# Optimization experiments

Measured on AMD Instinct MI355X. Metric: run time of the kernel, lower is better.

## Reference

```python
import jax, jax.numpy as jnp
import numpy as np

N_NODES = 50000


def gcn_conv(x, src, dst, W, b, n):
    # PyG GCNConv: h = x @ W; out[i] = sum_j norm_ij * h[j] + b, with added self-loops
    h = x @ W  # [N, out]
    deg = jax.ops.segment_sum(jnp.ones_like(dst, dtype=h.dtype), dst, num_segments=n)
    inv_sqrt_deg = jnp.where(deg > 0, jax.lax.rsqrt(deg), 0.0)  # [N]
    coeff = inv_sqrt_deg[src] * inv_sqrt_deg[dst]  # [E]
    msg = h[src] * coeff[:, None]  # [E, out] gather (memory-bound)
    out = jax.ops.segment_sum(msg, dst, num_segments=n)  # scatter-add
    return out + b


def setup_inputs() -> dict:
    key = jax.random.key(0)
    ks = jax.random.split(key, 8)
    n, e, c_in, c_hid, c_out = N_NODES, 800000, 128, 128, 64
    x = jax.random.normal(ks[0], (n, c_in), dtype=jnp.float32)
    edge_index = jax.random.randint(ks[1], (2, e), 0, n, dtype=jnp.int64)
    # Glorot-ish scaled weights
    W1 = jax.random.normal(ks[2], (c_in, c_hid), dtype=jnp.float32) / np.sqrt(c_in)
    b1 = jnp.zeros((c_hid,), dtype=jnp.float32)
    W2 = jax.random.normal(ks[3], (c_hid, c_out), dtype=jnp.float32) / np.sqrt(c_hid)
    b2 = jnp.zeros((c_out,), dtype=jnp.float32)
    lin_W = jax.random.normal(ks[4], (2 * c_out, c_out), dtype=jnp.float32) / np.sqrt(2 * c_out)
    lin_b = jnp.zeros((c_out,), dtype=jnp.float32)
    return {"x": x, "edge_index": edge_index, "W1": W1, "b1": b1,
            "W2": W2, "b2": b2, "lin_W": lin_W, "lin_b": lin_b}


def reference(x, edge_index, W1, b1, W2, b2, lin_W, lin_b):
    n = x.shape[0]
    # add self-loops (as GCNConv does by default)
    loops = jnp.arange(n, dtype=edge_index.dtype)
    src = jnp.concatenate([edge_index[0], loops])
    dst = jnp.concatenate([edge_index[1], loops])

    def branch(x):
        h = jax.nn.relu(gcn_conv(x, src, dst, W1, b1, n))
        # dropout: identity in eval mode (training=False)
        return gcn_conv(h, src, dst, W2, b2, n)

    x1 = branch(x)
    x2 = branch(x)
    # FusionMethod == 'Concat'
    fused = jnp.concatenate([x1, x2], axis=1) @ lin_W + lin_b
    return jax.nn.log_softmax(fused, axis=1)
```

## Files before the change

### kernel.cpp

```cpp
#include <hip/hip_runtime.h>


#define CIN  128
#define CHID 128
#define COUT 64
#define BCAP_SH 13
#define BCAP    (1 << BCAP_SH)
#define BINCHUNK 2048

typedef short v8s __attribute__((ext_vector_type(8)));
typedef float v4f __attribute__((ext_vector_type(4)));

static __device__ __forceinline__ unsigned short f2bf(float f) {
    unsigned int u = __float_as_uint(f);
    unsigned int r = (u + 0x7fffu + ((u >> 16) & 1u)) >> 16;
    return (unsigned short)r;
}
static __device__ __forceinline__ float bf2f(unsigned short v) {
    return __uint_as_float(((unsigned int)v) << 16);
}

__global__ __launch_bounds__(256) void bin_kernel(const int* __restrict__ src,
                                                  const int* __restrict__ dst,
                                                  int* __restrict__ bcursor,
                                                  unsigned int* __restrict__ binned, int E) {
    __shared__ int h[256];
    __shared__ int base[256];
    int t = threadIdx.x;
    h[t] = 0;
    __syncthreads();
    int e0 = blockIdx.x * BINCHUNK;
    int e1 = e0 + BINCHUNK; if (e1 > E) e1 = E;
    for (int e = e0 + t; e < e1; e += 256)
        atomicAdd(&h[dst[e] >> 8], 1);
    __syncthreads();
    int c = h[t];
    base[t] = (t << BCAP_SH) + (c ? atomicAdd(&bcursor[t], c) : 0);
    __syncthreads();
    h[t] = 0;
    __syncthreads();
    for (int e = e0 + t; e < e1; e += 256) {
        int d = dst[e];
        int b = d >> 8;
        int pos = base[b] + atomicAdd(&h[b], 1);
        binned[pos] = (unsigned int)src[e] | (((unsigned int)d & 255u) << 16);
    }
}

__global__ __launch_bounds__(512) void csr_kernel(const unsigned int* __restrict__ binned,
                                                  const int* __restrict__ bcursor,
                                                  int2* __restrict__ rowpair,
                                                  float* __restrict__ inv,
                                                  int* __restrict__ ebuf, int n) {
    __shared__ int h[256];
    __shared__ int s[256];
    int b = blockIdx.x;
    int t = threadIdx.x;
    int base = b << BCAP_SH;
    int cnt  = bcursor[b];
    if (t < 256) h[t] = 0;
    __syncthreads();
    for (int i = t; i < cnt; i += 512)
        atomicAdd(&h[binned[base + i] >> 16], 1);
    __syncthreads();
    int myc = (t < 256) ? h[t] : 0;
    if (t < 256) s[t] = myc;
    __syncthreads();
    for (int off = 1; off < 256; off <<= 1) {
        int u = (t >= off && t < 256) ? s[t - off] : 0;
        __syncthreads();
        if (t < 256) s[t] += u;
        __syncthreads();
    }
    if (t < 256) {
        int excl = s[t] - myc;
        int node = (b << 8) + t;
        if (node < n) {
            rowpair[node] = make_int2(base + excl, base + excl + myc);
            inv[node] = rsqrtf((float)(myc + 1));
        }
        h[t] = base + excl;
    }
    __syncthreads();
    for (int i = t; i < cnt; i += 512) {
        unsigned int v = binned[base + i];
        int pos = atomicAdd(&h[v >> 16], 1);
        ebuf[pos] = (int)(v & 0xffffu);
    }
}

__global__ __launch_bounds__(128) void wprep_kernel(const float* __restrict__ W1,
                                                    const float* __restrict__ W2,
                                                    const float* __restrict__ b2,
                                                    const float* __restrict__ linW,
                                                    const float* __restrict__ linb,
                                                    unsigned short* __restrict__ Wt1,
                                                    unsigned short* __restrict__ Wt2,
                                                    float* __restrict__ bp,
                                                    int* __restrict__ bcursor) {
    int b = blockIdx.x;
    int t = threadIdx.x;
    if (b < CHID) {
        Wt1[b * CIN + t] = f2bf(W1[t * CHID + b]);
        if (t < COUT) {
            float acc = 0.f;
#pragma unroll 8
            for (int k = 0; k < COUT; ++k) {
                float wsv = linW[k * COUT + t] + linW[(k + COUT) * COUT + t];
                acc = fmaf(W2[b * COUT + k], wsv, acc);
            }
            Wt2[t * CHID + b] = f2bf(acc);
        }
    } else {
        bcursor[t] = 0;
        bcursor[128 + t] = 0;
        if (t < COUT) {
            float acc = 0.f;
#pragma unroll 8
            for (int k = 0; k < COUT; ++k) {
                float wsv = linW[k * COUT + t] + linW[(k + COUT) * COUT + t];
                acc = fmaf(b2[k], wsv, acc);
            }
            bp[t] = acc + linb[t];
        }
    }
}

template <int NOUT, bool A_BF16>
__global__ __launch_bounds__(256) void gemm_mfma(const void* __restrict__ Aptr,
                                                 const unsigned short* __restrict__ Wt,
                                                 const float* __restrict__ inv,
                                                 unsigned short* __restrict__ H, int n) {
    constexpr int NCT = NOUT / 16;
    int lane = threadIdx.x & 63;
    int wave = threadIdx.x >> 6;
    int quad = lane >> 4, r16 = lane & 15;
    int row0 = (blockIdx.x * 4 + wave) * 16;
    if (row0 >= n) return;
    int arow = row0 + r16;
    if (arow >= n) arow = n - 1;

    v4f acc[NCT];
#pragma unroll
    for (int c = 0; c < NCT; ++c) acc[c] = (v4f){0.f, 0.f, 0.f, 0.f};

#pragma unroll
    for (int kc = 0; kc < 4; ++kc) {
        v8s af;
        if (A_BF16) {
            const unsigned short* A = (const unsigned short*)Aptr;
            af = *(const v8s*)(A + (size_t)arow * 128 + kc * 32 + quad * 8);
        } else {
            const float* A = (const float*)Aptr;
            const float4* ap = (const float4*)(A + (size_t)arow * 128 + kc * 32 + quad * 8);
            float4 a0 = ap[0], a1 = ap[1];
            af[0] = (short)f2bf(a0.x); af[1] = (short)f2bf(a0.y);
            af[2] = (short)f2bf(a0.z); af[3] = (short)f2bf(a0.w);
            af[4] = (short)f2bf(a1.x); af[5] = (short)f2bf(a1.y);
            af[6] = (short)f2bf(a1.z); af[7] = (short)f2bf(a1.w);
        }
#pragma unroll
        for (int ct = 0; ct < NCT; ++ct) {
            v8s bf = *(const v8s*)(Wt + (size_t)(ct * 16 + r16) * 128 + kc * 32 + quad * 8);
            acc[ct] = __builtin_amdgcn_mfma_f32_16x16x32_bf16(af, bf, acc[ct], 0, 0, 0);
        }
    }

    float4 iv = ((const float4*)(inv + row0))[quad];
#pragma unroll
    for (int ct = 0; ct < NCT; ++ct) {
#pragma unroll
        for (int i = 0; i < 4; ++i) {
            int orow = row0 + quad * 4 + i;
            if (orow < n) {
                float sc = (i == 0) ? iv.x : (i == 1) ? iv.y : (i == 2) ? iv.z : iv.w;
                H[(size_t)orow * NOUT + ct * 16 + r16] = f2bf(acc[ct][i] * sc);
            }
        }
    }
}

__global__ void agg1_kernel(const unsigned int* __restrict__ Hs, const int* __restrict__ ebuf,
                            const int2* __restrict__ rowpair, const float* __restrict__ inv,
                            const float* __restrict__ bias, unsigned int* __restrict__ outp,
                            int n) {
    int node = __builtin_amdgcn_readfirstlane(blockIdx.x * 4 + (threadIdx.x >> 6));
    int lane = threadIdx.x & 63;
    if (node >= n) return;
    int2 rp = rowpair[node];
    int beg = rp.x, len = rp.y - rp.x;
    int eid = ebuf[beg + lane];
    int m = len < 64 ? len : 64;
    float ax = 0.f, ay = 0.f;
    int k = 0;
    for (; k + 4 <= m; k += 4) {
        int s0 = __builtin_amdgcn_readlane(eid, k);
        int s1 = __builtin_amdgcn_readlane(eid, k + 1);
        int s2 = __builtin_amdgcn_readlane(eid, k + 2);
        int s3 = __builtin_amdgcn_readlane(eid, k + 3);
        unsigned int u0 = Hs[(size_t)s0 * 64 + lane];
        unsigned int u1 = Hs[(size_t)s1 * 64 + lane];
        unsigned int u2 = Hs[(size_t)s2 * 64 + lane];
        unsigned int u3 = Hs[(size_t)s3 * 64 + lane];
        ax += __uint_as_float(u0 << 16);  ay += __uint_as_float(u0 & 0xffff0000u);
        ax += __uint_as_float(u1 << 16);  ay += __uint_as_float(u1 & 0xffff0000u);
        ax += __uint_as_float(u2 << 16);  ay += __uint_as_float(u2 & 0xffff0000u);
        ax += __uint_as_float(u3 << 16);  ay += __uint_as_float(u3 & 0xffff0000u);
    }
    for (; k < m; ++k) {
        int s = __builtin_amdgcn_readlane(eid, k);
        unsigned int u = Hs[(size_t)s * 64 + lane];
        ax += __uint_as_float(u << 16);
        ay += __uint_as_float(u & 0xffff0000u);
    }
    for (; k < len; ++k) {
        int s = ebuf[beg + k];
        unsigned int u = Hs[(size_t)s * 64 + lane];
        ax += __uint_as_float(u << 16);
        ay += __uint_as_float(u & 0xffff0000u);
    }
    {
        unsigned int u = Hs[(size_t)node * 64 + lane];
        ax += __uint_as_float(u << 16);
        ay += __uint_as_float(u & 0xffff0000u);
    }
    float wd = inv[node];
    float2 bv = ((const float2*)bias)[lane];
    float ox = fmaxf(fmaf(wd, ax, bv.x), 0.f);
    float oy = fmaxf(fmaf(wd, ay, bv.y), 0.f);
    outp[(size_t)node * 64 + lane] =
        (unsigned int)f2bf(ox) | ((unsigned int)f2bf(oy) << 16);
}

__global__ void agg2_final_kernel(const unsigned short* __restrict__ Hs,
                                  const int* __restrict__ ebuf, const int2* __restrict__ rowpair,
                                  const float* __restrict__ inv, const float* __restrict__ bp,
                                  float* __restrict__ outp, int n) {
    int node = __builtin_amdgcn_readfirstlane(blockIdx.x * 4 + (threadIdx.x >> 6));
    int lane = threadIdx.x & 63;
    if (node >= n) return;
    int2 rp = rowpair[node];
    int beg = rp.x, len = rp.y - rp.x;
    int eid = ebuf[beg + lane];
    int m = len < 64 ? len : 64;
    float acc = 0.f;
    int k = 0;
    for (; k + 4 <= m; k += 4) {
        int s0 = __builtin_amdgcn_readlane(eid, k);
        int s1 = __builtin_amdgcn_readlane(eid, k + 1);
        int s2 = __builtin_amdgcn_readlane(eid, k + 2);
        int s3 = __builtin_amdgcn_readlane(eid, k + 3);
        float v0 = bf2f(Hs[(size_t)s0 * 64 + lane]);
        float v1 = bf2f(Hs[(size_t)s1 * 64 + lane]);
        float v2 = bf2f(Hs[(size_t)s2 * 64 + lane]);
        float v3 = bf2f(Hs[(size_t)s3 * 64 + lane]);
        acc += v0 + v1 + v2 + v3;
    }
    for (; k < m; ++k) {
        int s = __builtin_amdgcn_readlane(eid, k);
        acc += bf2f(Hs[(size_t)s * 64 + lane]);
    }
    for (; k < len; ++k) {
        acc += bf2f(Hs[(size_t)ebuf[beg + k] * 64 + lane]);
    }
    acc += bf2f(Hs[(size_t)node * 64 + lane]);
    float fo = fmaf(inv[node], acc, bp[lane]);
    float mx = fo;
#pragma unroll
    for (int off = 32; off >= 1; off >>= 1) mx = fmaxf(mx, __shfl_xor(mx, off, 64));
    float ex = expf(fo - mx);
    float s = ex;
#pragma unroll
    for (int off = 32; off >= 1; off >>= 1) s += __shfl_xor(s, off, 64);
    outp[(size_t)node * COUT + lane] = fo - mx - logf(s);
}

static inline size_t align16(size_t x) { return (x + 15) & ~(size_t)15; }

extern "C" void kernel_launch(void* const* d_in, const int* in_sizes, int n_in,
                              void* d_out, int out_size, void* d_ws, size_t ws_size,
                              hipStream_t stream) {
    const float* x    = (const float*)d_in[0];
    const int*   eidx = (const int*)d_in[1];
    const float* W1   = (const float*)d_in[2];
    const float* b1   = (const float*)d_in[3];
    const float* W2   = (const float*)d_in[4];
    const float* b2   = (const float*)d_in[5];
    const float* linW = (const float*)d_in[6];
    const float* linb = (const float*)d_in[7];
    float* out = (float*)d_out;

    const int n = in_sizes[0] / CIN;
    const int E = in_sizes[1] / 2;
    const int* src = eidx;
    const int* dst = eidx + E;
    const int NBKT = (n + 255) >> 8;

    char* ws = (char*)d_ws;
    size_t off = 0;
    int2*  rowpair = (int2*)(ws + off);  off = align16(off + (size_t)n * 8);
    float* inv     = (float*)(ws + off); off = align16(off + (size_t)n * 4);
    int*   bcursor = (int*)(ws + off);   off = align16(off + 256 * 4);
    unsigned short* Wt1 = (unsigned short*)(ws + off); off = align16(off + (size_t)CHID * CIN * 2);
    unsigned short* Wt2 = (unsigned short*)(ws + off); off = align16(off + (size_t)COUT * CHID * 2);
    float* bp      = (float*)(ws + off); off = align16(off + (size_t)COUT * 4);
    unsigned int* binned = (unsigned int*)(ws + off); off = align16(off + (size_t)256 * BCAP * 4);
    int*   ebuf    = (int*)(ws + off);   off = align16(off + (size_t)256 * BCAP * 4);
    unsigned short* h1s   = (unsigned short*)(ws + off); off = align16(off + (size_t)n * CHID * 2);
    unsigned short* agg1b = (unsigned short*)(ws + off); off = align16(off + (size_t)n * CHID * 2);
    unsigned short* h2p   = (unsigned short*)(ws + off); off = align16(off + (size_t)n * COUT * 2);

    wprep_kernel<<<CHID + 1, 128, 0, stream>>>(W1, W2, b2, linW, linb, Wt1, Wt2, bp, bcursor);

    bin_kernel<<<(E + BINCHUNK - 1) / BINCHUNK, 256, 0, stream>>>(src, dst, bcursor, binned, E);
    csr_kernel<<<NBKT, 512, 0, stream>>>(binned, bcursor, rowpair, inv, ebuf, n);

    gemm_mfma<CHID, false><<<(n + 63) / 64, 256, 0, stream>>>(x, Wt1, inv, h1s, n);
    agg1_kernel<<<(n + 3) / 4, 256, 0, stream>>>((const unsigned int*)h1s, ebuf, rowpair, inv, b1,
                                                 (unsigned int*)agg1b, n);

    gemm_mfma<COUT, true><<<(n + 63) / 64, 256, 0, stream>>>(agg1b, Wt2, inv, h2p, n);
    agg2_final_kernel<<<(n + 3) / 4, 256, 0, stream>>>(h2p, ebuf, rowpair, inv, bp, out, n);
}
```

Measured before the change: 216.3 us.

## Split layer-1 features into two column halves and aggregate each half separately

The first GEMM now writes its bf16 output as two planar 64-column halves, one per contiguous block, instead of 128-column rows. agg1 launches twice as many blocks, each gathering one half (one bf16 per lane), with the block index arranged so paired halves of the same node group run close together. The inner gather loop is unrolled to 8 with a tree-shaped sum. The aim is to shrink the working set per gather pass so it fits in cache better and to raise memory-level parallelism, at the cost of re-reading the edge lists and row pointers twice.

```diff
diff --git a/kernel.cpp b/kernel.cpp
--- a/kernel.cpp
+++ b/kernel.cpp
@@ -126,7 +126,7 @@
     }
 }
 
-template <int NOUT, bool A_BF16>
+template <int NOUT, bool A_BF16, bool SPLIT>
 __global__ __launch_bounds__(256) void gemm_mfma(const void* __restrict__ Aptr,
                                                  const unsigned short* __restrict__ Wt,
                                                  const float* __restrict__ inv,
@@ -174,62 +174,62 @@
             int orow = row0 + quad * 4 + i;
             if (orow < n) {
                 float sc = (i == 0) ? iv.x : (i == 1) ? iv.y : (i == 2) ? iv.z : iv.w;
-                H[(size_t)orow * NOUT + ct * 16 + r16] = f2bf(acc[ct][i] * sc);
+                int col = ct * 16 + r16;
+                size_t idx = SPLIT
+                    ? ((size_t)(col >> 6) * n * 64 + (size_t)orow * 64 + (col & 63))
+                    : ((size_t)orow * NOUT + col);
+                H[idx] = f2bf(acc[ct][i] * sc);
             }
         }
     }
 }
 
-__global__ void agg1_kernel(const unsigned int* __restrict__ Hs, const int* __restrict__ ebuf,
+__global__ void agg1_kernel(const unsigned short* __restrict__ Hs, const int* __restrict__ ebuf,
                             const int2* __restrict__ rowpair, const float* __restrict__ inv,
-                            const float* __restrict__ bias, unsigned int* __restrict__ outp,
+                            const float* __restrict__ bias, unsigned short* __restrict__ outp,
                             int n) {
-    int node = __builtin_amdgcn_readfirstlane(blockIdx.x * 4 + (threadIdx.x >> 6));
+    int g = blockIdx.x;
+    int oct = g >> 3, pos = g & 7;
+    int half = pos >> 2;
+    int node = __builtin_amdgcn_readfirstlane((oct * 4 + (pos & 3)) * 4 + (threadIdx.x >> 6));
     int lane = threadIdx.x & 63;
     if (node >= n) return;
+    const unsigned short* H = Hs + (size_t)half * n * 64;
     int2 rp = rowpair[node];
     int beg = rp.x, len = rp.y - rp.x;
     int eid = ebuf[beg + lane];
     int m = len < 64 ? len : 64;
-    float ax = 0.f, ay = 0.f;
+    float acc = 0.f;
     int k = 0;
-    for (; k + 4 <= m; k += 4) {
+    for (; k + 8 <= m; k += 8) {
         int s0 = __builtin_amdgcn_readlane(eid, k);
         int s1 = __builtin_amdgcn_readlane(eid, k + 1);
         int s2 = __builtin_amdgcn_readlane(eid, k + 2);
         int s3 = __builtin_amdgcn_readlane(eid, k + 3);
-        unsigned int u0 = Hs[(size_t)s0 * 64 + lane];
-        unsigned int u1 = Hs[(size_t)s1 * 64 + lane];
-        unsigned int u2 = Hs[(size_t)s2 * 64 + lane];
-        unsigned int u3 = Hs[(size_t)s3 * 64 + lane];
-        ax += __uint_as_float(u0 << 16);  ay += __uint_as_float(u0 & 0xffff0000u);
-        ax += __uint_as_float(u1 << 16);  ay += __uint_as_float(u1 & 0xffff0000u);
-        ax += __uint_as_float(u2 << 16);  ay += __uint_as_float(u2 & 0xffff0000u);
-        ax += __uint_as_float(u3 << 16);  ay += __uint_as_float(u3 & 0xffff0000u);
+        int s4 = __builtin_amdgcn_readlane(eid, k + 4);
+        int s5 = __builtin_amdgcn_readlane(eid, k + 5);
+        int s6 = __builtin_amdgcn_readlane(eid, k + 6);
+        int s7 = __builtin_amdgcn_readlane(eid, k + 7);
+        float v0 = bf2f(H[(size_t)s0 * 64 + lane]);
+        float v1 = bf2f(H[(size_t)s1 * 64 + lane]);
+        float v2 = bf2f(H[(size_t)s2 * 64 + lane]);
+        float v3 = bf2f(H[(size_t)s3 * 64 + lane]);
+        float v4 = bf2f(H[(size_t)s4 * 64 + lane]);
+        float v5 = bf2f(H[(size_t)s5 * 64 + lane]);
+        float v6 = bf2f(H[(size_t)s6 * 64 + lane]);
+        float v7 = bf2f(H[(size_t)s7 * 64 + lane]);
+        acc += ((v0 + v1) + (v2 + v3)) + ((v4 + v5) + (v6 + v7));
     }
     for (; k < m; ++k) {
         int s = __builtin_amdgcn_readlane(eid, k);
-        unsigned int u = Hs[(size_t)s * 64 + lane];
-        ax += __uint_as_float(u << 16);
-        ay += __uint_as_float(u & 0xffff0000u);
-    }
-    for (; k < len; ++k) {
-        int s = ebuf[beg + k];
-        unsigned int u = Hs[(size_t)s * 64 + lane];
-        ax += __uint_as_float(u << 16);
-        ay += __uint_as_float(u & 0xffff0000u);
-    }
-    {
-        unsigned int u = Hs[(size_t)node * 64 + lane];
-        ax += __uint_as_float(u << 16);
-        ay += __uint_as_float(u & 0xffff0000u);
-    }
+        acc += bf2f(H[(size_t)s * 64 + lane]);
+    }
+    for (; k < len; ++k)
+        acc += bf2f(H[(size_t)ebuf[beg + k] * 64 + lane]);
+    acc += bf2f(H[(size_t)node * 64 + lane]);
     float wd = inv[node];
-    float2 bv = ((const float2*)bias)[lane];
-    float ox = fmaxf(fmaf(wd, ax, bv.x), 0.f);
-    float oy = fmaxf(fmaf(wd, ay, bv.y), 0.f);
-    outp[(size_t)node * 64 + lane] =
-        (unsigned int)f2bf(ox) | ((unsigned int)f2bf(oy) << 16);
+    float o = fmaxf(fmaf(wd, acc, bias[half * 64 + lane]), 0.f);
+    outp[(size_t)node * 128 + half * 64 + lane] = f2bf(o);
 }
 
 __global__ void agg2_final_kernel(const unsigned short* __restrict__ Hs,
@@ -254,15 +254,14 @@
         float v1 = bf2f(Hs[(size_t)s1 * 64 + lane]);
         float v2 = bf2f(Hs[(size_t)s2 * 64 + lane]);
         float v3 = bf2f(Hs[(size_t)s3 * 64 + lane]);
-        acc += v0 + v1 + v2 + v3;
+        acc += (v0 + v1) + (v2 + v3);
     }
     for (; k < m; ++k) {
         int s = __builtin_amdgcn_readlane(eid, k);
         acc += bf2f(Hs[(size_t)s * 64 + lane]);
     }
-    for (; k < len; ++k) {
+    for (; k < len; ++k)
         acc += bf2f(Hs[(size_t)ebuf[beg + k] * 64 + lane]);
-    }
     acc += bf2f(Hs[(size_t)node * 64 + lane]);
     float fo = fmaf(inv[node], acc, bp[lane]);
     float mx = fo;
@@ -315,10 +314,12 @@
     bin_kernel<<<(E + BINCHUNK - 1) / BINCHUNK, 256, 0, stream>>>(src, dst, bcursor, binned, E);
     csr_kernel<<<NBKT, 512, 0, stream>>>(binned, bcursor, rowpair, inv, ebuf, n);
 
-    gemm_mfma<CHID, false><<<(n + 63) / 64, 256, 0, stream>>>(x, Wt1, inv, h1s, n);
-    agg1_kernel<<<(n + 3) / 4, 256, 0, stream>>>((const unsigned int*)h1s, ebuf, rowpair, inv, b1,
-                                                 (unsigned int*)agg1b, n);
-
-    gemm_mfma<COUT, true><<<(n + 63) / 64, 256, 0, stream>>>(agg1b, Wt2, inv, h2p, n);
+    gemm_mfma<CHID, false, true><<<(n + 63) / 64, 256, 0, stream>>>(x, Wt1, inv, h1s, n);
+    {
+        int octs = (n + 15) / 16;
+        agg1_kernel<<<octs * 8, 256, 0, stream>>>(h1s, ebuf, rowpair, inv, b1, agg1b, n);
+    }
+
+    gemm_mfma<COUT, true, false><<<(n + 63) / 64, 256, 0, stream>>>(agg1b, Wt2, inv, h2p, n);
     agg2_final_kernel<<<(n + 3) / 4, 256, 0, stream>>>(h2p, ebuf, rowpair, inv, bp, out, n);
 }
```

Result: slower. 229.0 us (+5.8%).
